# Kernel tuning notes

Hardware: AMD Instinct MI355X
Metric: run time of the kernel (lower is better)

Reference implementation:

```python
import jax, jax.numpy as jnp
import numpy as np

E, H, V = 512, 1024, 50257
NUM_STEPS = 19  # range(1, 20) in the original loop


def setup_inputs() -> dict:
    key = jax.random.key(0)
    ks = jax.random.split(key, 8)
    s = 0.02  # small init so sigmoids/tanh stay in a sane range
    return {
        "inp": jax.random.normal(ks[0], (1, 1, E), dtype=jnp.float32),
        "W_ih": jax.random.normal(ks[1], (4 * H, E), dtype=jnp.float32) * s,
        "W_hh": jax.random.normal(ks[2], (4 * H, H), dtype=jnp.float32) * s,
        "b_ih": jax.random.normal(ks[3], (4 * H,), dtype=jnp.float32) * s,
        "b_hh": jax.random.normal(ks[4], (4 * H,), dtype=jnp.float32) * s,
        "emb": jax.random.normal(ks[5], (V, E), dtype=jnp.float32) * s,
        "W_lin": jax.random.normal(ks[6], (V, H), dtype=jnp.float32) * s,
        "b_lin": jax.random.normal(ks[7], (V,), dtype=jnp.float32) * s,
    }


def reference(inp, W_ih, W_hh, b_ih, b_hh, emb, W_lin, b_lin):
    # inp: [1, 1, E] (batch_first single timestep); states=None -> zero h/c
    x0 = inp[:, 0, :]                      # [1, E]
    h0 = jnp.zeros((1, H), dtype=inp.dtype)
    c0 = jnp.zeros((1, H), dtype=inp.dtype)

    def step(carry, _):
        x, h, c = carry
        # torch LSTM gate order: i, f, g, o
        gates = x @ W_ih.T + b_ih + h @ W_hh.T + b_hh   # [1, 4H]
        i, f, g, o = jnp.split(gates, 4, axis=-1)
        i = jax.nn.sigmoid(i)
        f = jax.nn.sigmoid(f)
        g = jnp.tanh(g)
        o = jax.nn.sigmoid(o)
        c = f * c + i * g
        h = o * jnp.tanh(c)
        logits = h @ W_lin.T + b_lin                    # [1, V]
        tok = jnp.argmax(logits, axis=-1)               # [1] greedy token
        x_next = emb[tok]                               # [1, E] embedding lookup
        return (x_next, h, c), tok[0]

    _, toks = jax.lax.scan(step, (x0, h0, c0), None, length=NUM_STEPS)
    return toks  # [19] int token ids, same as the Python list of .item()s
```

## Files before the change

### kernel.cpp

```cpp
#include <hip/hip_runtime.h>
#include <hip/hip_bf16.h>
#include <math.h>

#define E_DIM 512
#define H_DIM 1024
#define V_DIM 50257
#define NSTEPS 19
#define NB_F32 1024
#define NB_LOG 256
#define RPW 13
#define RPB 208
#define VPAD 53248
#define NB_GATES 256
#define BL_CAP 192
#define CAND_CAP 1024
#define PF 4

#define OFF_X      0
#define OFF_H      4096
#define OFF_C      8192
#define OFF_C2     12288
#define OFF_GATES  16384
#define OFF_HN     32768
#define OFF_PART   33024
#define OFF_PBLOCK 41216
#define OFF_SNB    49152
#define OFF_LE     901120
#define OFF_WBI    1327104
#define WS_NEEDED  55853056ull

__device__ inline unsigned fmap(float f) {
    unsigned u = __float_as_uint(f);
    return (u & 0x80000000u) ? ~u : (u | 0x80000000u);
}
__device__ inline unsigned long long packmax(float s, int row) {
    return ((unsigned long long)fmap(s) << 32) | (unsigned)(0xFFFFFFFFu - (unsigned)row);
}
__device__ inline float sigm(float v) { return 1.0f / (1.0f + expf(-v)); }

__device__ inline void load_h4(const float* __restrict__ h, float4 hr[4], int lane) {
    const float4* h4 = (const float4*)h;
#pragma unroll
    for (int j = 0; j < 4; ++j) hr[j] = h4[lane + 64 * j];
}
__device__ inline float row_dot4(const float* __restrict__ Wrow,
                                 const float4 hr[4], int lane) {
    const float4* w4 = (const float4*)Wrow;
    float s = 0.f;
#pragma unroll
    for (int j = 0; j < 4; ++j) {
        float4 w = w4[lane + 64 * j];
        s = fmaf(w.x, hr[j].x, s); s = fmaf(w.y, hr[j].y, s);
        s = fmaf(w.z, hr[j].z, s); s = fmaf(w.w, hr[j].w, s);
    }
#pragma unroll
    for (int off = 32; off; off >>= 1) s += __shfl_xor(s, off, 64);
    return s;
}

__global__ void init_kernel(const float* __restrict__ inp,
                            float* __restrict__ x, float* __restrict__ h,
                            float* __restrict__ c, float4* __restrict__ SNB) {
    int i = threadIdx.x;
    if (i < E_DIM) x[i] = inp[i];
    h[i] = 0.f; c[i] = 0.f;
    for (int p = i; p < VPAD - V_DIM; p += 1024)
        SNB[V_DIM + p] = make_float4(0.f, 0.f, -1e30f, 0.f);
}

__global__ void gatesfin_kernel(const float* __restrict__ Wih,
                                const float* __restrict__ Whh,
                                const float* __restrict__ bih,
                                const float* __restrict__ bhh,
                                const float* __restrict__ xg,
                                const float* __restrict__ h,
                                float* __restrict__ gates,
                                const float2* __restrict__ LE,
                                const float2* __restrict__ pblock,
                                const float* __restrict__ Wlin,
                                const float* __restrict__ blin,
                                const float* __restrict__ emb,
                                int* __restrict__ tok_out, int doFin) {
    const int tid = threadIdx.x, lane = tid & 63, wave = tid >> 6;

    float4 hr[4];
    load_h4(h, hr, lane);

    __shared__ float s_wmx[4];
    __shared__ float s_M;
    __shared__ int s_nb, s_nc, s_ovf;
    __shared__ int s_blist[BL_CAP];
    __shared__ int s_clist[CAND_CAP];
    __shared__ unsigned long long s_bp[4];
    __shared__ int s_tok;

    float4 xr[2];
    if (doFin) {
        float2 pb = pblock[tid];
        float m = pb.x;
#pragma unroll
        for (int off = 32; off; off >>= 1) m = fmaxf(m, __shfl_xor(m, off, 64));
        if (lane == 0) s_wmx[wave] = m;
        __syncthreads();
        if (tid == 0) {
            s_M = fmaxf(fmaxf(s_wmx[0], s_wmx[1]), fmaxf(s_wmx[2], s_wmx[3]));
            s_nb = 0; s_nc = 0; s_ovf = 0;
        }
        __syncthreads();
        const float M = s_M;
        if (pb.y >= M) { int p = atomicAdd(&s_nb, 1); if (p < BL_CAP) s_blist[p] = tid; else s_ovf = 1; }
        __syncthreads();
        if (!s_ovf) {
            int nb = s_nb < BL_CAP ? s_nb : BL_CAP;
            for (int ii = tid; ii < nb * RPB; ii += 256) {
                int bi = ii / RPB, off = ii - bi * RPB;
                int r = s_blist[bi] * RPB + off;
                float2 le = LE[r];
                if (le.x + le.y >= M) {
                    int p = atomicAdd(&s_nc, 1);
                    if (p < CAND_CAP) s_clist[p] = r; else s_ovf = 1;
                }
            }
        }
        __syncthreads();
        if (tid == 0 && s_nc == 0) s_ovf = 1;
        __syncthreads();
        const int ovf = s_ovf;
        const int n = s_nc < CAND_CAP ? s_nc : CAND_CAP;

        unsigned long long bestp = 0ull;
        if (!ovf) {
            for (int ci = wave; ci < n; ci += 4) {
                int row = s_clist[ci];
                float s = row_dot4(Wlin + (size_t)row * H_DIM, hr, lane) + blin[row];
                unsigned long long p = packmax(s, row);
                if (p > bestp) bestp = p;
            }
        } else {
            for (int row = wave; row < V_DIM; row += 4) {
                float s = row_dot4(Wlin + (size_t)row * H_DIM, hr, lane) + blin[row];
                unsigned long long p = packmax(s, row);
                if (p > bestp) bestp = p;
            }
        }
        if (lane == 0) s_bp[wave] = bestp;
        __syncthreads();
        if (tid == 0) {
            unsigned long long B = s_bp[0];
            for (int w = 1; w < 4; ++w) if (s_bp[w] > B) B = s_bp[w];
            int tok = (int)(0xFFFFFFFFu - (unsigned)(B & 0xFFFFFFFFu));
            s_tok = tok;
            *tok_out = tok;
        }
        __syncthreads();
        int tokc = s_tok;
        if (tokc < 0) tokc = 0;
        if (tokc >= V_DIM) tokc = V_DIM - 1;
        const float4* e4 = (const float4*)(emb + (size_t)tokc * E_DIM);
        xr[0] = e4[lane]; xr[1] = e4[lane + 64];
    } else {
        const float4* x4 = (const float4*)xg;
        xr[0] = x4[lane]; xr[1] = x4[lane + 64];
    }

    for (int row = blockIdx.x * 4 + wave; row < 4 * H_DIM; row += NB_GATES * 4) {
        const float4* wi = (const float4*)(Wih + (size_t)row * E_DIM);
        const float4* wh = (const float4*)(Whh + (size_t)row * H_DIM);
        float s = 0.f;
#pragma unroll
        for (int j = 0; j < 2; ++j) {
            float4 w = wi[lane + j * 64];
            s = fmaf(w.x, xr[j].x, s); s = fmaf(w.y, xr[j].y, s);
            s = fmaf(w.z, xr[j].z, s); s = fmaf(w.w, xr[j].w, s);
        }
#pragma unroll
        for (int j = 0; j < 4; ++j) {
            float4 w = wh[lane + j * 64];
            s = fmaf(w.x, hr[j].x, s); s = fmaf(w.y, hr[j].y, s);
            s = fmaf(w.z, hr[j].z, s); s = fmaf(w.w, hr[j].w, s);
        }
#pragma unroll
        for (int off = 32; off; off >>= 1) s += __shfl_xor(s, off, 64);
        if (lane == 0) gates[row] = s + bih[row] + bhh[row];
    }
}

__global__ void cell_kernel(const float* __restrict__ gates,
                            float* __restrict__ c, float* __restrict__ h,
                            float* __restrict__ hn) {
    int j = threadIdx.x;
    float iv = sigm(gates[j]);
    float fv = sigm(gates[j + H_DIM]);
    float gv = tanhf(gates[j + 2 * H_DIM]);
    float ov = sigm(gates[j + 3 * H_DIM]);
    float cv = fv * c[j] + iv * gv;
    c[j] = cv;
    float hv = ov * tanhf(cv);
    h[j] = hv;

    float sq = hv * hv;
#pragma unroll
    for (int off = 32; off; off >>= 1) sq += __shfl_xor(sq, off, 64);
    __shared__ float ws[16];
    int lane = j & 63, wv = j >> 6;
    if (lane == 0) ws[wv] = sq;
    __syncthreads();
    if (j == 0) {
        float t = 0.f;
        for (int w = 0; w < 16; ++w) t += ws[w];
        *hn = sqrtf(t);
    }
}

__global__ void logits_f32_kernel(const float* __restrict__ Wlin,
                                  const float* __restrict__ blin,
                                  const float* __restrict__ h,
                                  uint4* __restrict__ WbI,
                                  float4* __restrict__ SNB, int doConv,
                                  unsigned long long* __restrict__ partials) {
    const int tid = threadIdx.x, lane = tid & 63, wave = tid >> 6;
    const int gw = blockIdx.x * 4 + wave;

    float4 hr[4];
    load_h4(h, hr, lane);

    float best = -INFINITY;
    int bidx = 0x7fffffff;
    for (int row = gw; row < V_DIM; row += NB_F32 * 4) {
        const float4* w4 = (const float4*)(Wlin + (size_t)row * H_DIM);
        float4 A[4];
#pragma unroll
        for (int j = 0; j < 4; ++j) A[j] = w4[lane + 64 * j];

        float s = 0.f, mx = 0.f;
#pragma unroll
        for (int j = 0; j < 4; ++j) {
            s = fmaf(A[j].x, hr[j].x, s); s = fmaf(A[j].y, hr[j].y, s);
            s = fmaf(A[j].z, hr[j].z, s); s = fmaf(A[j].w, hr[j].w, s);
            mx = fmaxf(mx, fmaxf(fmaxf(fabsf(A[j].x), fabsf(A[j].y)),
                                 fmaxf(fabsf(A[j].z), fabsf(A[j].w))));
        }
#pragma unroll
        for (int off = 32; off; off >>= 1) {
            s += __shfl_xor(s, off, 64);
            mx = fmaxf(mx, __shfl_xor(mx, off, 64));
        }

        if (doConv) {
            float scale = mx * (1.0f / 127.0f);
            float inv = (mx > 0.f) ? (127.0f / mx) : 0.f;
            float d2 = 0.f;
            unsigned pw[4];
#pragma unroll
            for (int j = 0; j < 4; ++j) {
                float q0 = fminf(fmaxf(rintf(A[j].x * inv), -127.f), 127.f);
                float q1 = fminf(fmaxf(rintf(A[j].y * inv), -127.f), 127.f);
                float q2 = fminf(fmaxf(rintf(A[j].z * inv), -127.f), 127.f);
                float q3 = fminf(fmaxf(rintf(A[j].w * inv), -127.f), 127.f);
                float r0 = A[j].x - q0 * scale;
                float r1 = A[j].y - q1 * scale;
                float r2 = A[j].z - q2 * scale;
                float r3 = A[j].w - q3 * scale;
                d2 = fmaf(r0, r0, d2); d2 = fmaf(r1, r1, d2);
                d2 = fmaf(r2, r2, d2); d2 = fmaf(r3, r3, d2);
                pw[j] = ((unsigned)(int)q0 & 0xFFu) | (((unsigned)(int)q1 & 0xFFu) << 8) |
                        (((unsigned)(int)q2 & 0xFFu) << 16) | (((unsigned)(int)q3 & 0xFFu) << 24);
            }
#pragma unroll
            for (int off = 32; off; off >>= 1) d2 += __shfl_xor(d2, off, 64);
            WbI[(size_t)row * 64 + lane] = make_uint4(pw[0], pw[1], pw[2], pw[3]);
            if (lane == 0)
                SNB[row] = make_float4(scale, sqrtf(d2) + 3e-3f * mx, blin[row], 0.f);
        }
        s += blin[row];
        if (s > best) { best = s; bidx = row; }
    }

    __shared__ float bv[4];
    __shared__ int bi[4];
    if (lane == 0) { bv[wave] = best; bi[wave] = bidx; }
    __syncthreads();
    if (tid == 0) {
        float B = bv[0]; int I = bi[0];
        for (int w = 1; w < 4; ++w)
            if (bv[w] > B || (bv[w] == B && bi[w] < I)) { B = bv[w]; I = bi[w]; }
        partials[blockIdx.x] = packmax(B, I);
    }
}

__global__ void finalize_f32_kernel(const unsigned long long* __restrict__ partials,
                                    const float* __restrict__ emb,
                                    float* __restrict__ x, int* __restrict__ tok_out) {
    const int lane = threadIdx.x & 63, wave = threadIdx.x >> 6;
    unsigned long long best = 0ull;
    for (int i = threadIdx.x; i < NB_F32; i += 256) {
        unsigned long long p = partials[i];
        if (p > best) best = p;
    }
#pragma unroll
    for (int off = 32; off; off >>= 1) {
        unsigned long long o = __shfl_xor(best, off, 64);
        if (o > best) best = o;
    }
    __shared__ unsigned long long sb[4];
    __shared__ int stok;
    if (lane == 0) sb[wave] = best;
    __syncthreads();
    if (threadIdx.x == 0) {
        unsigned long long B = sb[0];
        for (int w = 1; w < 4; ++w) if (sb[w] > B) B = sb[w];
        int tok = (int)(0xFFFFFFFFu - (unsigned)(B & 0xFFFFFFFFu));
        *tok_out = tok;
        stok = tok;
    }
    __syncthreads();
    int tok = stok;
    if (tok < 0) tok = 0;
    if (tok >= V_DIM) tok = V_DIM - 1;
    const float4* e4 = (const float4*)(emb + (size_t)tok * E_DIM);
    float4* x4 = (float4*)x;
    if (threadIdx.x < E_DIM / 4) x4[threadIdx.x] = e4[threadIdx.x];
}

__global__ void logits_i8_kernel(const uint4* __restrict__ WbI,
                                 const float4* __restrict__ SNB,
                                 const float* __restrict__ gates,
                                 const float* __restrict__ cin,
                                 float* __restrict__ cout,
                                 float* __restrict__ hout,
                                 float2* __restrict__ LE,
                                 float2* __restrict__ pblock) {
    const int tid = threadIdx.x, lane = tid & 63, wave = tid >> 6;
    const int wid = blockIdx.x * 16 + wave;
    const int r0 = wid * RPW;

    const uint4* rb = WbI + (size_t)r0 * 64 + lane;
    uint4 wq[RPW];
#pragma unroll
    for (int k = 0; k < PF; ++k) wq[k] = rb[(size_t)k * 64];

    __shared__ float h_lds[H_DIM];
    __shared__ float cpart[4];

    if (wave < 4) {
        const int idx4 = wave * 64 + lane;
        const float4* g4i = (const float4*)gates;
        const float4* g4f = (const float4*)(gates + H_DIM);
        const float4* g4g = (const float4*)(gates + 2 * H_DIM);
        const float4* g4o = (const float4*)(gates + 3 * H_DIM);
        const float4* c4  = (const float4*)cin;
        float4 gi = g4i[idx4], gf = g4f[idx4], gg = g4g[idx4], go = g4o[idx4], cc = c4[idx4];
        float4 hv, cv;
        cv.x = sigm(gf.x) * cc.x + sigm(gi.x) * tanhf(gg.x);
        cv.y = sigm(gf.y) * cc.y + sigm(gi.y) * tanhf(gg.y);
        cv.z = sigm(gf.z) * cc.z + sigm(gi.z) * tanhf(gg.z);
        cv.w = sigm(gf.w) * cc.w + sigm(gi.w) * tanhf(gg.w);
        hv.x = sigm(go.x) * tanhf(cv.x);
        hv.y = sigm(go.y) * tanhf(cv.y);
        hv.z = sigm(go.z) * tanhf(cv.z);
        hv.w = sigm(go.w) * tanhf(cv.w);
        ((float4*)h_lds)[idx4] = hv;
        if (blockIdx.x == 0) {
            ((float4*)hout)[idx4] = hv;
            ((float4*)cout)[idx4] = cv;
        }
        float sq = fmaf(hv.x, hv.x, fmaf(hv.y, hv.y, fmaf(hv.z, hv.z, hv.w * hv.w)));
#pragma unroll
        for (int off = 32; off; off >>= 1) sq += __shfl_xor(sq, off, 64);
        if (lane == 0) cpart[wave] = sq;
    }
    __syncthreads();
    const float K = sqrtf(cpart[0] + cpart[1] + cpart[2] + cpart[3]);

    float4 hr[4];
#pragma unroll
    for (int j = 0; j < 4; ++j) hr[j] = ((const float4*)h_lds)[lane + 64 * j];

    float maxl = -INFINITY, maxu = -INFINITY;
#pragma unroll
    for (int k = 0; k < RPW; ++k) {
        if (k + PF < RPW) wq[k + PF] = rb[(size_t)(k + PF) * 64];
        uint4 c = wq[k];
        float s = 0.f;
        {
            int v = (int)c.x;
            s = fmaf((float)((v << 24) >> 24), hr[0].x, s);
            s = fmaf((float)((v << 16) >> 24), hr[0].y, s);
            s = fmaf((float)((v << 8) >> 24),  hr[0].z, s);
            s = fmaf((float)(v >> 24),         hr[0].w, s);
        }
        {
            int v = (int)c.y;
            s = fmaf((float)((v << 24) >> 24), hr[1].x, s);
            s = fmaf((float)((v << 16) >> 24), hr[1].y, s);
            s = fmaf((float)((v << 8) >> 24),  hr[1].z, s);
            s = fmaf((float)(v >> 24),         hr[1].w, s);
        }
        {
            int v = (int)c.z;
            s = fmaf((float)((v << 24) >> 24), hr[2].x, s);
            s = fmaf((float)((v << 16) >> 24), hr[2].y, s);
            s = fmaf((float)((v << 8) >> 24),  hr[2].z, s);
            s = fmaf((float)(v >> 24),         hr[2].w, s);
        }
        {
            int v = (int)c.w;
            s = fmaf((float)((v << 24) >> 24), hr[3].x, s);
            s = fmaf((float)((v << 16) >> 24), hr[3].y, s);
            s = fmaf((float)((v << 8) >> 24),  hr[3].z, s);
            s = fmaf((float)(v >> 24),         hr[3].w, s);
        }
#pragma unroll
        for (int off = 32; off; off >>= 1) s += __shfl_xor(s, off, 64);
        int r = r0 + k;
        float4 snb = SNB[r];
        float L = fmaf(snb.x, s, snb.z);
        float e = fmaf(snb.y, K, 1e-6f);
        if (lane == 0) LE[r] = make_float2(L, e);
        maxl = fmaxf(maxl, L - e);
        maxu = fmaxf(maxu, L + e);
    }

    __shared__ float wl[16], wu[16];
    if (lane == 0) { wl[wave] = maxl; wu[wave] = maxu; }
    __syncthreads();
    if (tid == 0) {
        float lo = wl[0], up = wu[0];
        for (int w = 1; w < 16; ++w) { lo = fmaxf(lo, wl[w]); up = fmaxf(up, wu[w]); }
        pblock[blockIdx.x] = make_float2(lo, up);
    }
}

__global__ void finalize_tail_kernel(const float2* __restrict__ LE,
                                     const float2* __restrict__ pblock,
                                     const float* __restrict__ Wlin,
                                     const float* __restrict__ blin,
                                     const float* __restrict__ h,
                                     const float* __restrict__ emb,
                                     float* __restrict__ x, int* __restrict__ tok_out) {
    const int tid = threadIdx.x;
    const int lane = tid & 63, wv = tid >> 6;

    __shared__ float wmx[16];
    __shared__ float sM;
    __shared__ int snb, sncand, sovf;
    __shared__ int blist[BL_CAP];
    __shared__ int clist[CAND_CAP];

    float2 pb = make_float2(-INFINITY, -INFINITY);
    if (tid < NB_LOG) pb = pblock[tid];
    float m = pb.x;
#pragma unroll
    for (int off = 32; off; off >>= 1) m = fmaxf(m, __shfl_xor(m, off, 64));
    if (lane == 0) wmx[wv] = m;
    __syncthreads();
    if (tid == 0) {
        float M = wmx[0];
        for (int w = 1; w < 16; ++w) M = fmaxf(M, wmx[w]);
        sM = M; snb = 0; sncand = 0; sovf = 0;
    }
    __syncthreads();
    const float M = sM;

    if (tid < NB_LOG && pb.y >= M) {
        int p = atomicAdd(&snb, 1);
        if (p < BL_CAP) blist[p] = tid; else sovf = 1;
    }
    __syncthreads();
    if (!sovf) {
        int nb = snb < BL_CAP ? snb : BL_CAP;
        for (int ii = tid; ii < nb * RPB; ii += 1024) {
            int bi = ii / RPB, off = ii - bi * RPB;
            int r = blist[bi] * RPB + off;
            float2 le = LE[r];
            if (le.x + le.y >= M) {
                int p = atomicAdd(&sncand, 1);
                if (p < CAND_CAP) clist[p] = r; else sovf = 1;
            }
        }
    }
    __syncthreads();
    if (tid == 0 && sncand == 0) sovf = 1;
    __syncthreads();
    const int ovf = sovf;
    const int n = sncand < CAND_CAP ? sncand : CAND_CAP;

    float4 hr[4];
    load_h4(h, hr, lane);
    unsigned long long bestp = 0ull;
    if (!ovf) {
        for (int ci = wv; ci < n; ci += 16) {
            int row = clist[ci];
            float s = row_dot4(Wlin + (size_t)row * H_DIM, hr, lane) + blin[row];
            unsigned long long p = packmax(s, row);
            if (p > bestp) bestp = p;
        }
    } else {
        for (int row = wv; row < V_DIM; row += 16) {
            float s = row_dot4(Wlin + (size_t)row * H_DIM, hr, lane) + blin[row];
            unsigned long long p = packmax(s, row);
            if (p > bestp) bestp = p;
        }
    }
    __shared__ unsigned long long sbp[16];
    __shared__ int stok;
    if (lane == 0) sbp[wv] = bestp;
    __syncthreads();
    if (tid == 0) {
        unsigned long long B = sbp[0];
        for (int w = 1; w < 16; ++w) if (sbp[w] > B) B = sbp[w];
        int tok = (int)(0xFFFFFFFFu - (unsigned)(B & 0xFFFFFFFFu));
        stok = tok;
        *tok_out = tok;
    }
    __syncthreads();
    int tok = stok;
    if (tok < 0) tok = 0;
    if (tok >= V_DIM) tok = V_DIM - 1;
    const float4* e4 = (const float4*)(emb + (size_t)tok * E_DIM);
    float4* xo = (float4*)x;
    if (tid < E_DIM / 4) xo[tid] = e4[tid];
}

extern "C" void kernel_launch(void* const* d_in, const int* in_sizes, int n_in,
                              void* d_out, int out_size, void* d_ws, size_t ws_size,
                              hipStream_t stream) {
    const float* inp  = (const float*)d_in[0];
    const float* Wih  = (const float*)d_in[1];
    const float* Whh  = (const float*)d_in[2];
    const float* bih  = (const float*)d_in[3];
    const float* bhh  = (const float*)d_in[4];
    const float* emb  = (const float*)d_in[5];
    const float* Wlin = (const float*)d_in[6];
    const float* blin = (const float*)d_in[7];
    int* toks = (int*)d_out;

    char* ws = (char*)d_ws;
    float* x     = (float*)(ws + OFF_X);
    float* h     = (float*)(ws + OFF_H);
    float* c0b   = (float*)(ws + OFF_C);
    float* c1b   = (float*)(ws + OFF_C2);
    float* gates = (float*)(ws + OFF_GATES);
    float* hn    = (float*)(ws + OFF_HN);
    unsigned long long* partials = (unsigned long long*)(ws + OFF_PART);
    float2* pblock = (float2*)(ws + OFF_PBLOCK);
    float4* SNB  = (float4*)(ws + OFF_SNB);
    float2* LE   = (float2*)(ws + OFF_LE);
    uint4* WbI   = (uint4*)(ws + OFF_WBI);

    const int useI8 = (ws_size >= WS_NEEDED) ? 1 : 0;

    init_kernel<<<1, 1024, 0, stream>>>(inp, x, h, c0b, SNB);

    if (!useI8) {
        for (int step = 0; step < NSTEPS; ++step) {
            gatesfin_kernel<<<NB_GATES, 256, 0, stream>>>(
                Wih, Whh, bih, bhh, x, h, gates, LE, pblock, Wlin, blin, emb,
                (int*)nullptr, 0);
            cell_kernel<<<1, 1024, 0, stream>>>(gates, c0b, h, hn);
            logits_f32_kernel<<<NB_F32, 256, 0, stream>>>(
                Wlin, blin, h, WbI, SNB, 0, partials);
            finalize_f32_kernel<<<1, 256, 0, stream>>>(partials, emb, x, toks + step);
        }
        return;
    }

    gatesfin_kernel<<<NB_GATES, 256, 0, stream>>>(
        Wih, Whh, bih, bhh, x, h, gates, LE, pblock, Wlin, blin, emb,
        (int*)nullptr, 0);
    cell_kernel<<<1, 1024, 0, stream>>>(gates, c0b, h, hn);
    logits_f32_kernel<<<NB_F32, 256, 0, stream>>>(
        Wlin, blin, h, WbI, SNB, 1, partials);
    finalize_f32_kernel<<<1, 256, 0, stream>>>(partials, emb, x, toks + 0);

    for (int t = 1; t < NSTEPS; ++t) {
        gatesfin_kernel<<<NB_GATES, 256, 0, stream>>>(
            Wih, Whh, bih, bhh, x, h, gates, LE, pblock, Wlin, blin, emb,
            (t >= 2) ? (toks + t - 1) : (int*)nullptr, (t >= 2) ? 1 : 0);
        float* cin  = (t & 1) ? c0b : c1b;
        float* cout = (t & 1) ? c1b : c0b;
        logits_i8_kernel<<<NB_LOG, 1024, 0, stream>>>(
            WbI, SNB, gates, cin, cout, h, LE, pblock);
    }
    finalize_tail_kernel<<<1, 1024, 0, stream>>>(LE, pblock, Wlin, blin, h, emb,
                                                 x, toks + NSTEPS - 1);
}
```

Baseline: 435.9 us.

## Transpose int8 logits weights so each lane owns a row, split K across waves

```diff
diff --git a/kernel.cpp b/kernel.cpp
--- a/kernel.cpp
+++ b/kernel.cpp
@@ -7,14 +7,12 @@
 #define V_DIM 50257
 #define NSTEPS 19
 #define NB_F32 1024
-#define NB_LOG 256
-#define RPW 13
-#define RPB 208
+#define NB_LOG 416
+#define RPB 128
 #define VPAD 53248
 #define NB_GATES 256
-#define BL_CAP 192
+#define BL_CAP 256
 #define CAND_CAP 1024
-#define PF 4
 
 #define OFF_X      0
 #define OFF_H      4096
@@ -26,7 +24,7 @@
 #define OFF_PBLOCK 41216
 #define OFF_SNB    49152
 #define OFF_LE     901120
-#define OFF_WBI    1327104
+#define OFF_WBT    1327104
 #define WS_NEEDED  55853056ull
 
 __device__ inline unsigned fmap(float f) {
@@ -96,8 +94,10 @@
 
     float4 xr[2];
     if (doFin) {
-        float2 pb = pblock[tid];
-        float m = pb.x;
+        float2 pb0 = pblock[tid];
+        float2 pb1 = (tid + 256 < NB_LOG) ? pblock[tid + 256]
+                                          : make_float2(-INFINITY, -INFINITY);
+        float m = fmaxf(pb0.x, pb1.x);
 #pragma unroll
         for (int off = 32; off; off >>= 1) m = fmaxf(m, __shfl_xor(m, off, 64));
         if (lane == 0) s_wmx[wave] = m;
@@ -108,12 +108,13 @@
         }
         __syncthreads();
         const float M = s_M;
-        if (pb.y >= M) { int p = atomicAdd(&s_nb, 1); if (p < BL_CAP) s_blist[p] = tid; else s_ovf = 1; }
+        if (pb0.y >= M) { int p = atomicAdd(&s_nb, 1); if (p < BL_CAP) s_blist[p] = tid; else s_ovf = 1; }
+        if (pb1.y >= M) { int p = atomicAdd(&s_nb, 1); if (p < BL_CAP) s_blist[p] = tid + 256; else s_ovf = 1; }
         __syncthreads();
         if (!s_ovf) {
             int nb = s_nb < BL_CAP ? s_nb : BL_CAP;
             for (int ii = tid; ii < nb * RPB; ii += 256) {
-                int bi = ii / RPB, off = ii - bi * RPB;
+                int bi = ii >> 7, off = ii & 127;
                 int r = s_blist[bi] * RPB + off;
                 float2 le = LE[r];
                 if (le.x + le.y >= M) {
@@ -215,7 +216,7 @@
 __global__ void logits_f32_kernel(const float* __restrict__ Wlin,
                                   const float* __restrict__ blin,
                                   const float* __restrict__ h,
-                                  uint4* __restrict__ WbI,
+                                  unsigned* __restrict__ WbT,
                                   float4* __restrict__ SNB, int doConv,
                                   unsigned long long* __restrict__ partials) {
     const int tid = threadIdx.x, lane = tid & 63, wave = tid >> 6;
@@ -268,7 +269,14 @@
             }
 #pragma unroll
             for (int off = 32; off; off >>= 1) d2 += __shfl_xor(d2, off, 64);
-            WbI[(size_t)row * 64 + lane] = make_uint4(pw[0], pw[1], pw[2], pw[3]);
+            {
+                size_t gb = (size_t)(row >> 6) * 16384 + (size_t)(row & 63) * 4;
+#pragma unroll
+                for (int j = 0; j < 4; ++j) {
+                    int cb = lane + 64 * j;
+                    WbT[gb + (size_t)(cb >> 2) * 256 + (cb & 3)] = pw[j];
+                }
+            }
             if (lane == 0)
                 SNB[row] = make_float4(scale, sqrtf(d2) + 3e-3f * mx, blin[row], 0.f);
         }
@@ -322,25 +330,28 @@
     if (threadIdx.x < E_DIM / 4) x4[threadIdx.x] = e4[threadIdx.x];
 }
 
-__global__ void logits_i8_kernel(const uint4* __restrict__ WbI,
-                                 const float4* __restrict__ SNB,
-                                 const float* __restrict__ gates,
-                                 const float* __restrict__ cin,
-                                 float* __restrict__ cout,
-                                 float* __restrict__ hout,
-                                 float2* __restrict__ LE,
-                                 float2* __restrict__ pblock) {
+__global__ __launch_bounds__(512)
+void logits_i8t_kernel(const uint4* __restrict__ WbT4,
+                       const float4* __restrict__ SNB,
+                       const float* __restrict__ gates,
+                       const float* __restrict__ cin,
+                       float* __restrict__ cout,
+                       float* __restrict__ hout,
+                       float2* __restrict__ LE,
+                       float2* __restrict__ pblock) {
     const int tid = threadIdx.x, lane = tid & 63, wave = tid >> 6;
-    const int wid = blockIdx.x * 16 + wave;
-    const int r0 = wid * RPW;
-
-    const uint4* rb = WbI + (size_t)r0 * 64 + lane;
-    uint4 wq[RPW];
-#pragma unroll
-    for (int k = 0; k < PF; ++k) wq[k] = rb[(size_t)k * 64];
+    const int g = blockIdx.x * 2 + (wave >> 2);
+    const int q = wave & 3;
+    const uint4* base = WbT4 + (size_t)g * 4096 + (size_t)q * 1024 + lane;
+
+    uint4 wq[16];
+#pragma unroll
+    for (int i = 0; i < 8; ++i) wq[i] = base[i * 64];
 
     __shared__ float h_lds[H_DIM];
     __shared__ float cpart[4];
+    __shared__ float part[8][64];
+    __shared__ float wl[2], wu[2];
 
     if (wave < 4) {
         const int idx4 = wave * 64 + lane;
@@ -372,63 +383,62 @@
     __syncthreads();
     const float K = sqrtf(cpart[0] + cpart[1] + cpart[2] + cpart[3]);
 
-    float4 hr[4];
-#pragma unroll
-    for (int j = 0; j < 4; ++j) hr[j] = ((const float4*)h_lds)[lane + 64 * j];
-
-    float maxl = -INFINITY, maxu = -INFINITY;
-#pragma unroll
-    for (int k = 0; k < RPW; ++k) {
-        if (k + PF < RPW) wq[k + PF] = rb[(size_t)(k + PF) * 64];
-        uint4 c = wq[k];
-        float s = 0.f;
-        {
-            int v = (int)c.x;
-            s = fmaf((float)((v << 24) >> 24), hr[0].x, s);
-            s = fmaf((float)((v << 16) >> 24), hr[0].y, s);
-            s = fmaf((float)((v << 8) >> 24),  hr[0].z, s);
-            s = fmaf((float)(v >> 24),         hr[0].w, s);
-        }
-        {
-            int v = (int)c.y;
-            s = fmaf((float)((v << 24) >> 24), hr[1].x, s);
-            s = fmaf((float)((v << 16) >> 24), hr[1].y, s);
-            s = fmaf((float)((v << 8) >> 24),  hr[1].z, s);
-            s = fmaf((float)(v >> 24),         hr[1].w, s);
-        }
-        {
-            int v = (int)c.z;
-            s = fmaf((float)((v << 24) >> 24), hr[2].x, s);
-            s = fmaf((float)((v << 16) >> 24), hr[2].y, s);
-            s = fmaf((float)((v << 8) >> 24),  hr[2].z, s);
-            s = fmaf((float)(v >> 24),         hr[2].w, s);
-        }
-        {
-            int v = (int)c.w;
-            s = fmaf((float)((v << 24) >> 24), hr[3].x, s);
-            s = fmaf((float)((v << 16) >> 24), hr[3].y, s);
-            s = fmaf((float)((v << 8) >> 24),  hr[3].z, s);
-            s = fmaf((float)(v >> 24),         hr[3].w, s);
-        }
-#pragma unroll
-        for (int off = 32; off; off >>= 1) s += __shfl_xor(s, off, 64);
-        int r = r0 + k;
+#pragma unroll
+    for (int i = 8; i < 16; ++i) wq[i] = base[i * 64];
+
+    const float4* hb = ((const float4*)h_lds) + q * 64;
+    float s = 0.f;
+#pragma unroll
+    for (int i = 0; i < 16; ++i) {
+        uint4 v = wq[i];
+        float4 h0 = hb[i * 4 + 0];
+        float4 h1 = hb[i * 4 + 1];
+        float4 h2 = hb[i * 4 + 2];
+        float4 h3 = hb[i * 4 + 3];
+        int a;
+        a = (int)v.x;
+        s = fmaf((float)((a << 24) >> 24), h0.x, s);
+        s = fmaf((float)((a << 16) >> 24), h0.y, s);
+        s = fmaf((float)((a << 8) >> 24),  h0.z, s);
+        s = fmaf((float)(a >> 24),         h0.w, s);
+        a = (int)v.y;
+        s = fmaf((float)((a << 24) >> 24), h1.x, s);
+        s = fmaf((float)((a << 16) >> 24), h1.y, s);
+        s = fmaf((float)((a << 8) >> 24),  h1.z, s);
+        s = fmaf((float)(a >> 24),         h1.w, s);
+        a = (int)v.z;
+        s = fmaf((float)((a << 24) >> 24), h2.x, s);
+        s = fmaf((float)((a << 16) >> 24), h2.y, s);
+        s = fmaf((float)((a << 8) >> 24),  h2.z, s);
+        s = fmaf((float)(a >> 24),         h2.w, s);
+        a = (int)v.w;
+        s = fmaf((float)((a << 24) >> 24), h3.x, s);
+        s = fmaf((float)((a << 16) >> 24), h3.y, s);
+        s = fmaf((float)((a << 8) >> 24),  h3.z, s);
+        s = fmaf((float)(a >> 24),         h3.w, s);
+    }
+    part[wave][lane] = s;
+    __syncthreads();
+
+    if (wave < 2) {
+        float st = part[wave * 4 + 0][lane] + part[wave * 4 + 1][lane] +
+                   part[wave * 4 + 2][lane] + part[wave * 4 + 3][lane];
+        int r = (blockIdx.x * 2 + wave) * 64 + lane;
         float4 snb = SNB[r];
-        float L = fmaf(snb.x, s, snb.z);
+        float L = fmaf(snb.x, st, snb.z);
         float e = fmaf(snb.y, K, 1e-6f);
-        if (lane == 0) LE[r] = make_float2(L, e);
-        maxl = fmaxf(maxl, L - e);
-        maxu = fmaxf(maxu, L + e);
-    }
-
-    __shared__ float wl[16], wu[16];
-    if (lane == 0) { wl[wave] = maxl; wu[wave] = maxu; }
-    __syncthreads();
-    if (tid == 0) {
-        float lo = wl[0], up = wu[0];
-        for (int w = 1; w < 16; ++w) { lo = fmaxf(lo, wl[w]); up = fmaxf(up, wu[w]); }
-        pblock[blockIdx.x] = make_float2(lo, up);
-    }
+        LE[r] = make_float2(L, e);
+        float lo = L - e, up = L + e;
+#pragma unroll
+        for (int off = 32; off; off >>= 1) {
+            lo = fmaxf(lo, __shfl_xor(lo, off, 64));
+            up = fmaxf(up, __shfl_xor(up, off, 64));
+        }
+        if (lane == 0) { wl[wave] = lo; wu[wave] = up; }
+    }
+    __syncthreads();
+    if (tid == 0)
+        pblock[blockIdx.x] = make_float2(fmaxf(wl[0], wl[1]), fmaxf(wu[0], wu[1]));
 }
 
 __global__ void finalize_tail_kernel(const float2* __restrict__ LE,
@@ -470,7 +480,7 @@
     if (!sovf) {
         int nb = snb < BL_CAP ? snb : BL_CAP;
         for (int ii = tid; ii < nb * RPB; ii += 1024) {
-            int bi = ii / RPB, off = ii - bi * RPB;
+            int bi = ii >> 7, off = ii & 127;
             int r = blist[bi] * RPB + off;
             float2 le = LE[r];
             if (le.x + le.y >= M) {
@@ -546,7 +556,7 @@
     float2* pblock = (float2*)(ws + OFF_PBLOCK);
     float4* SNB  = (float4*)(ws + OFF_SNB);
     float2* LE   = (float2*)(ws + OFF_LE);
-    uint4* WbI   = (uint4*)(ws + OFF_WBI);
+    unsigned* WbT = (unsigned*)(ws + OFF_WBT);
 
     const int useI8 = (ws_size >= WS_NEEDED) ? 1 : 0;
 
@@ -559,7 +569,7 @@
                 (int*)nullptr, 0);
             cell_kernel<<<1, 1024, 0, stream>>>(gates, c0b, h, hn);
             logits_f32_kernel<<<NB_F32, 256, 0, stream>>>(
-                Wlin, blin, h, WbI, SNB, 0, partials);
+                Wlin, blin, h, WbT, SNB, 0, partials);
             finalize_f32_kernel<<<1, 256, 0, stream>>>(partials, emb, x, toks + step);
         }
         return;
@@ -570,7 +580,7 @@
         (int*)nullptr, 0);
     cell_kernel<<<1, 1024, 0, stream>>>(gates, c0b, h, hn);
     logits_f32_kernel<<<NB_F32, 256, 0, stream>>>(
-        Wlin, blin, h, WbI, SNB, 1, partials);
+        Wlin, blin, h, WbT, SNB, 1, partials);
     finalize_f32_kernel<<<1, 256, 0, stream>>>(partials, emb, x, toks + 0);
 
     for (int t = 1; t < NSTEPS; ++t) {
@@ -579,8 +589,8 @@
             (t >= 2) ? (toks + t - 1) : (int*)nullptr, (t >= 2) ? 1 : 0);
         float* cin  = (t & 1) ? c0b : c1b;
         float* cout = (t & 1) ? c1b : c0b;
-        logits_i8_kernel<<<NB_LOG, 1024, 0, stream>>>(
-            WbI, SNB, gates, cin, cout, h, LE, pblock);
+        logits_i8t_kernel<<<NB_LOG, 512, 0, stream>>>(
+            (const uint4*)WbT, SNB, gates, cin, cout, h, LE, pblock);
     }
     finalize_tail_kernel<<<1, 1024, 0, stream>>>(LE, pblock, Wlin, blin, h, emb,
                                                  x, toks + NSTEPS - 1);
```

New measurement: 449.0 us. 1.03x slower.
